# Performance work log

Measured on AMD Instinct MI355X. Metric: run time of the kernel, lower is better.

Reference implementation:

```python
import jax, jax.numpy as jnp
import numpy as np

GROUPS = 8
EPS = 1e-5


def setup_inputs() -> dict:
    key = jax.random.key(0)
    k1, k2, k3 = jax.random.split(key, 3)
    B, C, H, W = 4, 256, 64, 64
    x = jax.random.normal(k1, (B, C, H, W), dtype=jnp.float32)
    gamma = jnp.ones((C,), dtype=jnp.float32)
    beta = jnp.zeros((C,), dtype=jnp.float32)
    # conv1x1 weights flattened to [out, in]
    w_qkv = jax.random.normal(k2, (3 * C, C), dtype=jnp.float32) * (C ** -0.5)
    w_proj = jax.random.normal(k3, (C, C), dtype=jnp.float32) * (C ** -0.5)
    b_proj = jnp.zeros((C,), dtype=jnp.float32)
    return {"x": x, "gamma": gamma, "beta": beta, "w_qkv": w_qkv,
            "w_proj": w_proj, "b_proj": b_proj}


def group_norm(x, gamma, beta):
    B, C, H, W = x.shape
    xr = x.reshape(B, GROUPS, C // GROUPS, H * W)
    mu = xr.mean(axis=(2, 3), keepdims=True)
    var = xr.var(axis=(2, 3), keepdims=True)
    xn = (xr - mu) * jax.lax.rsqrt(var + EPS)
    xn = xn.reshape(B, C, H * W)
    return xn * gamma[None, :, None] + beta[None, :, None]


def reference(x, gamma, beta, w_qkv, w_proj, b_proj):
    B, C, H, W = x.shape
    N = H * W
    xn = group_norm(x, gamma, beta)               # [B, C, N]
    qkv = jnp.einsum('oc,bcn->bon', w_qkv, xn)    # [B, 3C, N]
    q, k, v = jnp.split(qkv, 3, axis=1)           # each [B, C, N]
    # attn[b, n, m] = sum_c q[b,c,n] * k[b,c,m] * C^-0.5
    scores = jnp.einsum('bcn,bcm->bnm', q, k) * (C ** -0.5)  # [B, N, N]
    attn = jax.nn.softmax(scores, axis=-1)
    # out = v @ attn^T  -> out[b,c,n] = sum_m v[b,c,m] * attn[b,n,m]
    out = jnp.einsum('bcm,bnm->bcn', v, attn)     # [B, C, N]
    y = jnp.einsum('oc,bcn->bon', w_proj, out) + b_proj[None, :, None]
    return x + y.reshape(B, C, H, W)
```

## Files before the change

kernel.cpp:

```cpp
#include <hip/hip_runtime.h>
#include <hip/hip_bf16.h>

#define BB 4
#define CC 256
#define NN 4096
#define GG 8
#define SPLITS 4
#define TKV 32
#define ITERS (NN / SPLITS / TKV)

typedef unsigned char u8;
typedef unsigned short u16;
typedef unsigned int u32;
typedef __bf16 b16x8 __attribute__((ext_vector_type(8)));
typedef float f32x4 __attribute__((ext_vector_type(4)));
typedef u32 u32x4 __attribute__((ext_vector_type(4)));
typedef u32 u32x2 __attribute__((ext_vector_type(2)));
typedef u16 u16x4 __attribute__((ext_vector_type(4)));

#define QS 0.09016844005556021f
#define FMAX 8.0f


__device__ __forceinline__ u16 f2bf(float f) {
    u32 u = __builtin_bit_cast(u32, f);
    u = (u + 0x7FFFu + ((u >> 16) & 1u)) >> 16;
    return (u16)u;
}

__device__ __forceinline__ float bf2f(u16 h) {
    return __builtin_bit_cast(float, (u32)h << 16);
}

__device__ __forceinline__ u32 pack_bf2(float a, float b) {
    float2 f; f.x = a; f.y = b;
    __hip_bfloat162 h = __float22bfloat162_rn(f);
    u32 r;
    __builtin_memcpy(&r, &h, 4);
    return r;
}

__device__ __forceinline__ float exp2_raw(float x) {
#if __has_builtin(__builtin_amdgcn_exp2f)
    return __builtin_amdgcn_exp2f(x);
#else
    float r;
    asm("v_exp_f32 %0, %1" : "=v"(r) : "v"(x));
    return r;
#endif
}

__device__ __forceinline__ b16x8 ldfrag(const u16* p) {
    u32x4 v = *reinterpret_cast<const u32x4*>(p);
    return __builtin_bit_cast(b16x8, v);
}

__device__ __forceinline__ int pk_fp8x4(float a, float b, float c, float d) {
    int r = __builtin_amdgcn_cvt_pk_fp8_f32(a, b, 0, false);
    r = __builtin_amdgcn_cvt_pk_fp8_f32(c, d, r, true);
    return r;
}

__device__ __forceinline__ long as_long(u32x2 v) { return __builtin_bit_cast(long, v); }

__device__ __forceinline__ u32 swz16(u32 v) {
    return (u32)__builtin_amdgcn_ds_swizzle((int)v, 0x401F);
}

__device__ __forceinline__ void pls32(u32& a, u32& b) {
    asm("v_permlane32_swap_b32 %0, %1" : "+v"(a), "+v"(b));
}

typedef __attribute__((address_space(1))) const unsigned int* gas_p;
typedef __attribute__((address_space(3))) unsigned int* las_p;

__device__ __forceinline__ void g2l(const u8* g, u8* l) {
    __builtin_amdgcn_global_load_lds((gas_p)g, (las_p)l, 16, 0, 0);
}

__device__ __forceinline__ void g2l16(const u16* g, u16* l) {
    __builtin_amdgcn_global_load_lds((gas_p)g, (las_p)l, 16, 0, 0);
}

__global__ void fold_w(const float* __restrict__ w_qkv, const float* __restrict__ w_proj,
                       const float* __restrict__ gamma, const float* __restrict__ beta,
                       const float* __restrict__ gsum,
                       u16* __restrict__ wqf, float* __restrict__ biasq,
                       u16* __restrict__ wpf) {
    int o = blockIdx.x;
    int b = blockIdx.y;
    int c = threadIdx.x;
    int g = c >> 5;
    const float inv = 1.f / ((CC / GG) * NN);
    float s  = gsum[(b * GG + g) * 2];
    float ss = gsum[(b * GG + g) * 2 + 1];
    float mu = s * inv;
    float rstd = rsqrtf(ss * inv - mu * mu + 1e-5f);
    float a  = gamma[c] * rstd;
    float bb = beta[c] - mu * a;
    float w = w_qkv[o * CC + c];
    size_t fe = ((size_t)((o >> 4) * 8 + (c >> 5)) * 64 + ((c & 31) >> 3) * 16 + (o & 15)) * 8 + (c & 7);
    wqf[(size_t)b * 768 * CC + fe] = f2bf(w * a);
    float part = w * bb;
    #pragma unroll
    for (int off = 32; off; off >>= 1) part += __shfl_down(part, off, 64);
    __shared__ float red[4];
    if ((threadIdx.x & 63) == 0) red[threadIdx.x >> 6] = part;
    __syncthreads();
    if (threadIdx.x == 0) biasq[b * 768 + o] = red[0] + red[1] + red[2] + red[3];
    if (b == 0 && o < CC) {
        float wp = w_proj[o * CC + c];
        wpf[fe] = f2bf(wp);
    }
}

__global__ void transpose_x(const float* __restrict__ x, u16* __restrict__ xtf,
                            float* __restrict__ gsum) {
    __shared__ float tile[64][65];
    __shared__ float red[4][4];
    int n0 = blockIdx.x * 64, c0 = blockIdx.y * 64, b = blockIdx.z;
    int t = threadIdx.x;
    int c4 = (t & 15) * 4;
    int r0 = t >> 4;
    const float* xp = x + (size_t)b * CC * NN;
    float s0 = 0.f, ss0 = 0.f, s1 = 0.f, ss1 = 0.f;
    #pragma unroll
    for (int i = 0; i < 4; ++i) {
        int row = i * 16 + r0;
        float4 v = *reinterpret_cast<const float4*>(&xp[(size_t)(c0 + row) * NN + n0 + c4]);
        tile[row][c4 + 0] = v.x; tile[row][c4 + 1] = v.y;
        tile[row][c4 + 2] = v.z; tile[row][c4 + 3] = v.w;
        float s = v.x + v.y + v.z + v.w;
        float q = v.x * v.x + v.y * v.y + v.z * v.z + v.w * v.w;
        if (i < 2) { s0 += s; ss0 += q; } else { s1 += s; ss1 += q; }
    }
    #pragma unroll
    for (int off = 32; off; off >>= 1) {
        s0 += __shfl_down(s0, off, 64); ss0 += __shfl_down(ss0, off, 64);
        s1 += __shfl_down(s1, off, 64); ss1 += __shfl_down(ss1, off, 64);
    }
    int wid = t >> 6;
    if ((t & 63) == 0) { red[wid][0] = s0; red[wid][1] = ss0; red[wid][2] = s1; red[wid][3] = ss1; }
    __syncthreads();
    if (t < 2) {
        float s  = red[0][t * 2] + red[1][t * 2] + red[2][t * 2] + red[3][t * 2];
        float ss = red[0][t * 2 + 1] + red[1][t * 2 + 1] + red[2][t * 2 + 1] + red[3][t * 2 + 1];
        int g = (c0 >> 5) + t;
        atomicAdd(&gsum[(b * GG + g) * 2], s);
        atomicAdd(&gsum[(b * GG + g) * 2 + 1], ss);
    }
    int nl = t >> 2;
    int cbq = t & 3;
    int l15 = nl & 15;
    int ntile = (n0 >> 4) + (nl >> 4);
    int kk = (c0 >> 5) + (cbq >> 1);
    u16* ob = xtf + (size_t)b * NN * CC;
    #pragma unroll
    for (int g = 0; g < 4; ++g) {
        int quad = (cbq & 1) * 2 + (g >> 1);
        int j0 = (g & 1) * 4;
        u16x4 v;
        v.x = f2bf(tile[cbq * 16 + g * 4 + 0][nl]);
        v.y = f2bf(tile[cbq * 16 + g * 4 + 1][nl]);
        v.z = f2bf(tile[cbq * 16 + g * 4 + 2][nl]);
        v.w = f2bf(tile[cbq * 16 + g * 4 + 3][nl]);
        *reinterpret_cast<u16x4*>(ob + ((size_t)(ntile * 8 + kk) * 64 + quad * 16 + l15) * 8 + j0) = v;
    }
}

__global__ void __launch_bounds__(256) qkv_gemm(const u16* __restrict__ wqf,
                                                const float* __restrict__ biasq,
                                                const u16* __restrict__ xtf,
                                                u8* __restrict__ qtf, u8* __restrict__ ktf,
                                                u8* __restrict__ vvf) {
    __shared__ u16 bx[16384];
    int b = blockIdx.z;
    int o0 = blockIdx.y * 128;
    int n0 = blockIdx.x * 64;
    int lane = threadIdx.x & 63, w = threadIdx.x >> 6;
    int l15 = lane & 15, quad = lane >> 4;
    const u16* Bg = xtf + (size_t)b * NN * CC + (size_t)n0 * 256;
    #pragma unroll
    for (int j = 0; j < 8; ++j) {
        int c = w * 8 + j;
        g2l16(Bg + (size_t)c * 512 + lane * 8, bx + (size_t)c * 512 + lane * 8);
    }
    __syncthreads();

    const u16* A = wqf + (size_t)b * 768 * CC;
    f32x4 acc[2][4] = {};
    #pragma unroll
    for (int kk = 0; kk < 8; ++kk) {
        b16x8 af[2];
        #pragma unroll
        for (int t = 0; t < 2; ++t) {
            int otile = (o0 >> 4) + w * 2 + t;
            af[t] = ldfrag(A + (size_t)(otile * 8 + kk) * 512 + lane * 8);
        }
        #pragma unroll
        for (int nt = 0; nt < 4; ++nt) {
            b16x8 bf = ldfrag(bx + (size_t)(nt * 8 + kk) * 512 + lane * 8);
            acc[0][nt] = __builtin_amdgcn_mfma_f32_16x16x32_bf16(af[0], bf, acc[0][nt], 0, 0, 0);
            acc[1][nt] = __builtin_amdgcn_mfma_f32_16x16x32_bf16(af[1], bf, acc[1][nt], 0, 0, 0);
        }
    }
    #pragma unroll
    for (int t = 0; t < 2; ++t) {
        int o_base = o0 + (w * 2 + t) * 16 + quad * 4;
        float bias[4];
        #pragma unroll
        for (int r = 0; r < 4; ++r) bias[r] = biasq[b * 768 + o_base + r];
        if (o0 < 512) {
            int oloc = (o0 < 256) ? o_base : (o_base - 256);
            u8* dst = ((o0 < 256) ? qtf : ktf) + (size_t)b * NN * CC;
            #pragma unroll
            for (int nt = 0; nt < 4; ++nt) {
                int n = n0 + nt * 16 + l15;
                int pk = pk_fp8x4(acc[t][nt][0] + bias[0], acc[t][nt][1] + bias[1],
                                  acc[t][nt][2] + bias[2], acc[t][nt][3] + bias[3]);
                size_t addr = (size_t)((n >> 4) * 4 + (oloc >> 6)) * 1024
                            + ((oloc & 31) >> 3) * 256 + (n & 15) * 16
                            + ((oloc >> 5) & 1) * 8 + (oloc & 7);
                *reinterpret_cast<u32*>(dst + addr) = (u32)pk;
            }
        } else {
            int cb = o_base - 512;
            u8* dst = vvf + (size_t)b * NN * CC;
            #pragma unroll
            for (int nt = 0; nt < 4; ++nt) {
                int kv = n0 + nt * 16 + l15;
                int pk = pk_fp8x4(acc[t][nt][0] + bias[0], acc[t][nt][1] + bias[1],
                                  acc[t][nt][2] + bias[2], acc[t][nt][3] + bias[3]);
                size_t base = (size_t)((kv >> 5) * 8 + (cb >> 5)) * 1024
                            + ((kv & 31) >> 3) * 256 + ((cb >> 4) & 1) * 8 + (kv & 7);
                #pragma unroll
                for (int r = 0; r < 4; ++r)
                    dst[base + ((cb & 15) + r) * 16] = (u8)(pk >> (r * 8));
            }
        }
    }
}

__global__ void __launch_bounds__(256, 4) flash(const u8* __restrict__ qtf,
                                                const u8* __restrict__ ktf,
                                                const u8* __restrict__ vvf,
                                                u16* __restrict__ po,
                                                float* __restrict__ lp) {
    __shared__ u8 kbuf[2][8192];
    __shared__ u8 vbuf[2][8192];
    int lin = blockIdx.x;
    int chunk = lin & 15;
    int nblk = lin >> 4;
    int b = chunk >> 2, sp = chunk & 3;
    int lane = threadIdx.x & 63, w = threadIdx.x >> 6;
    int l15 = lane & 15, quad = lane >> 4;
    int ntile = nblk * 4 + w;
    const u8* kb8 = ktf + (size_t)b * NN * CC;
    const u8* vb8 = vvf + (size_t)b * NN * CC;
    const bool qodd = (quad & 1) != 0;

    u32x4 aq[4];
    const u8* qb = qtf + (size_t)b * NN * CC + (size_t)ntile * 4096;
    #pragma unroll
    for (int s = 0; s < 4; ++s)
        aq[s] = *reinterpret_cast<const u32x4*>(qb + s * 1024 + lane * 16);

    f32x4 acco[16] = {};
    f32x4 accs[2];
    const f32x4 zz = {0.f, 0.f, 0.f, 0.f};
    float lsum = 0.f;

    const int m_beg = sp * (NN / SPLITS);

    auto stage_k = [&](int buf, int m0) {
        const u8* ks = kb8 + ((size_t)m0 << 8);
        #pragma unroll
        for (int j = 0; j < 2; ++j) {
            int idx = w * 2 + j;
            g2l(ks + idx * 1024 + lane * 16, &kbuf[buf][idx * 1024]);
        }
    };
    auto stage_v = [&](int buf, int m0) {
        const u8* vs = vb8 + ((size_t)m0 << 8);
        #pragma unroll
        for (int j = 0; j < 2; ++j) {
            int idx = w * 2 + j;
            g2l(vs + idx * 1024 + lane * 16, &vbuf[buf][idx * 1024]);
        }
    };
    auto qk_tile = [&](const u8* kc) {
        __builtin_amdgcn_s_setprio(1);
        #pragma unroll
        for (int s = 0; s < 4; ++s) {
            long qlo = as_long(u32x2{aq[s].x, aq[s].y});
            long qhi = as_long(u32x2{aq[s].z, aq[s].w});
            #pragma unroll
            for (int mm = 0; mm < 2; ++mm) {
                u32x4 kf = *reinterpret_cast<const u32x4*>(kc + (size_t)(mm * 4 + s) * 1024 + lane * 16);
                accs[mm] = __builtin_amdgcn_mfma_f32_16x16x32_fp8_fp8(
                    as_long(u32x2{kf.x, kf.y}), qlo, (s == 0) ? zz : accs[mm], 0, 0, 0);
                accs[mm] = __builtin_amdgcn_mfma_f32_16x16x32_fp8_fp8(
                    as_long(u32x2{kf.z, kf.w}), qhi, accs[mm], 0, 0, 0);
            }
        }
        __builtin_amdgcn_s_setprio(0);
    };
    auto exch = [&](int pa, int pb) -> long {
        u32 a = (u32)pa, bm = (u32)pb;
        u32 ax = swz16(a), bx = swz16(bm);
        pls32(a, bm);
        pls32(ax, bx);
        u32 blo = qodd ? bx : a;
        u32 bhi = qodd ? bm : ax;
        return as_long(u32x2{blo, bhi});
    };

    stage_k(0, m_beg);
    stage_v(0, m_beg);
    stage_k(1, m_beg + TKV);
    __syncthreads();
    qk_tile(&kbuf[0][0]);
    __syncthreads();

    for (int it = 0; it < ITERS; ++it) {
        int cur = it & 1;
        int pk[2];
        #pragma unroll
        for (int mm = 0; mm < 2; ++mm) {
            float e0 = exp2_raw(fmaf(accs[mm][0], QS, -FMAX));
            float e1 = exp2_raw(fmaf(accs[mm][1], QS, -FMAX));
            float e2 = exp2_raw(fmaf(accs[mm][2], QS, -FMAX));
            float e3 = exp2_raw(fmaf(accs[mm][3], QS, -FMAX));
            lsum += (e0 + e1) + (e2 + e3);
            pk[mm] = pk_fp8x4(e0, e1, e2, e3);
        }
        if (it + 1 < ITERS) qk_tile(&kbuf[cur ^ 1][0]);
        if (it + 2 < ITERS) stage_k(cur, m_beg + (it + 2) * TKV);
        if (it + 1 < ITERS) stage_v(cur ^ 1, m_beg + (it + 1) * TKV);
        const u8* vc = &vbuf[cur][0];
        long bop = exch(pk[0], pk[1]);
        __builtin_amdgcn_s_setprio(1);
        #pragma unroll
        for (int c2 = 0; c2 < 8; ++c2) {
            u32x4 vf = *reinterpret_cast<const u32x4*>(vc + (size_t)c2 * 1024 + lane * 16);
            acco[c2 * 2]     = __builtin_amdgcn_mfma_f32_16x16x32_fp8_fp8(
                as_long(u32x2{vf.x, vf.y}), bop, acco[c2 * 2], 0, 0, 0);
            acco[c2 * 2 + 1] = __builtin_amdgcn_mfma_f32_16x16x32_fp8_fp8(
                as_long(u32x2{vf.z, vf.w}), bop, acco[c2 * 2 + 1], 0, 0, 0);
        }
        __builtin_amdgcn_s_setprio(0);
        __syncthreads();
    }
    u16* pochunk = po + ((size_t)(sp * BB + b) * 256 + ntile) * 4096;
    #pragma unroll
    for (int ct = 0; ct < 16; ++ct) {
        u32x2 st;
        st.x = pack_bf2(acco[ct][0], acco[ct][1]);
        st.y = pack_bf2(acco[ct][2], acco[ct][3]);
        *reinterpret_cast<u32x2*>(pochunk + (size_t)(ct * 64 + quad * 16 + l15) * 4) = st;
    }
    lsum += __shfl_xor(lsum, 16, 64);
    lsum += __shfl_xor(lsum, 32, 64);
    if (lane < 16)
        lp[(size_t)(sp * BB + b) * NN + ntile * 16 + l15] = lsum;
}

__global__ void __launch_bounds__(512) proj(const u16* __restrict__ wpf,
                                            const float* __restrict__ b_proj,
                                            const u16* __restrict__ po,
                                            const float* __restrict__ lp,
                                            const float* __restrict__ x,
                                            float* __restrict__ out) {
    __shared__ u16 bO[16384];
    int b = blockIdx.y, n0 = blockIdx.x * 64;
    int t = threadIdx.x;
    {
        int u = t & 127, ntl = t >> 7;
        int nb = (n0 >> 4) + ntl;
        int a = u & 7;
        int cblk = u >> 3;
        float accn[2][16] = {};
        float lsum2[2] = {};
        #pragma unroll
        for (int s = 0; s < SPLITS; ++s) {
            const u16* src = po + (((size_t)(s * BB + b) * 256 + nb) * 4096)
                           + cblk * 256 + a * 8;
            #pragma unroll
            for (int q4 = 0; q4 < 4; ++q4) {
                u16 s16[8];
                *reinterpret_cast<u32x4*>(s16) = *reinterpret_cast<const u32x4*>(src + q4 * 64);
                #pragma unroll
                for (int k = 0; k < 8; ++k)
                    accn[k >> 2][q4 * 4 + (k & 3)] += bf2f(s16[k]);
            }
            lsum2[0] += lp[(size_t)(s * BB + b) * NN + nb * 16 + a * 2];
            lsum2[1] += lp[(size_t)(s * BB + b) * NN + nb * 16 + a * 2 + 1];
        }
        #pragma unroll
        for (int nsel = 0; nsel < 2; ++nsel) {
            float inv = 1.f / lsum2[nsel];
            int row = a * 2 + nsel;
            #pragma unroll
            for (int h = 0; h < 2; ++h) {
                u16 outv[8];
                #pragma unroll
                for (int j = 0; j < 8; ++j) outv[j] = f2bf(accn[nsel][h * 8 + j] * inv);
                int kk = cblk >> 1, quad_f = (cblk & 1) * 2 + h;
                size_t off = ((size_t)(ntl * 8 + kk) * 64 + quad_f * 16 + row) * 8;
                *reinterpret_cast<u32x4*>(bO + off) = *reinterpret_cast<const u32x4*>(outv);
            }
        }
    }
    __syncthreads();
    int lane = t & 63, w = t >> 6;
    int l15 = lane & 15, quad = lane >> 4;
    f32x4 acc2[2][4] = {};
    #pragma unroll
    for (int kk = 0; kk < 8; ++kk) {
        b16x8 af[2];
        #pragma unroll
        for (int tt = 0; tt < 2; ++tt) {
            int otile = w * 2 + tt;
            af[tt] = ldfrag(wpf + (size_t)(otile * 8 + kk) * 512 + lane * 8);
        }
        #pragma unroll
        for (int nt = 0; nt < 4; ++nt) {
            b16x8 bf = ldfrag(bO + (size_t)(nt * 8 + kk) * 512 + lane * 8);
            acc2[0][nt] = __builtin_amdgcn_mfma_f32_16x16x32_bf16(af[0], bf, acc2[0][nt], 0, 0, 0);
            acc2[1][nt] = __builtin_amdgcn_mfma_f32_16x16x32_bf16(af[1], bf, acc2[1][nt], 0, 0, 0);
        }
    }
    #pragma unroll
    for (int tt = 0; tt < 2; ++tt) {
        int o_base = (w * 2 + tt) * 16 + quad * 4;
        #pragma unroll
        for (int nt = 0; nt < 4; ++nt) {
            int n = n0 + nt * 16 + l15;
            #pragma unroll
            for (int r = 0; r < 4; ++r) {
                int o = o_base + r;
                size_t idx = ((size_t)(b * CC + o)) * NN + n;
                out[idx] = acc2[tt][nt][r] + b_proj[o] + x[idx];
            }
        }
    }
}

extern "C" void kernel_launch(void* const* d_in, const int* in_sizes, int n_in,
                              void* d_out, int out_size, void* d_ws, size_t ws_size,
                              hipStream_t stream) {
    const float* x      = (const float*)d_in[0];
    const float* gamma  = (const float*)d_in[1];
    const float* beta   = (const float*)d_in[2];
    const float* w_qkv  = (const float*)d_in[3];
    const float* w_proj = (const float*)d_in[4];
    const float* b_proj = (const float*)d_in[5];
    float* out = (float*)d_out;

    char* p = (char*)d_ws;
    float* gsum  = (float*)p; p += 256;
    float* biasq = (float*)p; p += (size_t)BB * 768 * sizeof(float);
    u16* wqf = (u16*)p; p += (size_t)BB * 768 * CC * 2;
    u16* wpf = (u16*)p; p += (size_t)CC * CC * 2;
    u16* xtf = (u16*)p; p += (size_t)BB * NN * CC * 2;
    u8* qtf8 = (u8*)p; p += (size_t)BB * NN * CC;
    u8* ktf8 = (u8*)p; p += (size_t)BB * NN * CC;
    u8* vvf8 = (u8*)p; p += (size_t)BB * NN * CC;
    u16* po = (u16*)p; p += (size_t)SPLITS * BB * NN * CC * 2;
    float* lp = (float*)p; p += (size_t)SPLITS * BB * NN * sizeof(float);
    (void)ws_size; (void)in_sizes; (void)n_in; (void)out_size;

    (void)hipMemsetAsync(gsum, 0, BB * GG * 2 * sizeof(float), stream);
    transpose_x<<<dim3(NN / 64, CC / 64, BB), 256, 0, stream>>>(x, xtf, gsum);
    fold_w<<<dim3(768, BB), 256, 0, stream>>>(w_qkv, w_proj, gamma, beta, gsum, wqf, biasq, wpf);
    qkv_gemm<<<dim3(NN / 64, 6, BB), 256, 0, stream>>>(wqf, biasq, xtf, qtf8, ktf8, vvf8);
    flash<<<(NN / 64) * SPLITS * BB, 256, 0, stream>>>(qtf8, ktf8, vvf8, po, lp);
    proj<<<dim3(NN / 64, BB), 512, 0, stream>>>(wpf, b_proj, po, lp, x, out);
}
```

Before: 173.5 us.

## Use 16x16x128 scaled FP8 MFMA for QK scores with new Q/K layout

Replaces the sixteen 16x16x32 fp8 MFMAs per QK tile with four 16x16x128 f8f6f4 scaled MFMAs, with unit scales. The Q/K global layout written by the projection kernel changes so each lane reads 32 contiguous bytes per 128-channel chunk. The aim is fewer MFMA issues and higher MFMA throughput on gfx950. The new LDS read pattern (row stride 128 bytes) may cause bank conflicts.

```diff
diff --git a/kernel.cpp b/kernel.cpp
--- a/kernel.cpp
+++ b/kernel.cpp
@@ -17,6 +17,7 @@
 typedef u32 u32x4 __attribute__((ext_vector_type(4)));
 typedef u32 u32x2 __attribute__((ext_vector_type(2)));
 typedef u16 u16x4 __attribute__((ext_vector_type(4)));
+typedef int i32x8 __attribute__((ext_vector_type(8)));
 
 #define QS 0.09016844005556021f
 #define FMAX 8.0f
@@ -62,6 +63,17 @@
 }
 
 __device__ __forceinline__ long as_long(u32x2 v) { return __builtin_bit_cast(long, v); }
+
+__device__ __forceinline__ i32x8 cat8(u32x4 a, u32x4 b) {
+    i32x8 r;
+    r[0] = (int)a.x; r[1] = (int)a.y; r[2] = (int)a.z; r[3] = (int)a.w;
+    r[4] = (int)b.x; r[5] = (int)b.y; r[6] = (int)b.z; r[7] = (int)b.w;
+    return r;
+}
+
+__device__ __forceinline__ f32x4 mfma_qk128(i32x8 a, i32x8 b, f32x4 c) {
+    return __builtin_amdgcn_mfma_scale_f32_16x16x128_f8f6f4(a, b, c, 0, 0, 0, 127, 0, 127);
+}
 
 __device__ __forceinline__ u32 swz16(u32 v) {
     return (u32)__builtin_amdgcn_ds_swizzle((int)v, 0x401F);
@@ -218,9 +230,8 @@
                 int n = n0 + nt * 16 + l15;
                 int pk = pk_fp8x4(acc[t][nt][0] + bias[0], acc[t][nt][1] + bias[1],
                                   acc[t][nt][2] + bias[2], acc[t][nt][3] + bias[3]);
-                size_t addr = (size_t)((n >> 4) * 4 + (oloc >> 6)) * 1024
-                            + ((oloc & 31) >> 3) * 256 + (n & 15) * 16
-                            + ((oloc >> 5) & 1) * 8 + (oloc & 7);
+                size_t addr = (size_t)(n >> 4) * 4096 + (size_t)(oloc >> 7) * 2048
+                            + (size_t)(n & 15) * 128 + (oloc & 127);
                 *reinterpret_cast<u32*>(dst + addr) = (u32)pk;
             }
         } else {
@@ -259,11 +270,17 @@
     const u8* vb8 = vvf + (size_t)b * NN * CC;
     const bool qodd = (quad & 1) != 0;
 
-    u32x4 aq[4];
-    const u8* qb = qtf + (size_t)b * NN * CC + (size_t)ntile * 4096;
-    #pragma unroll
-    for (int s = 0; s < 4; ++s)
-        aq[s] = *reinterpret_cast<const u32x4*>(qb + s * 1024 + lane * 16);
+    i32x8 qop[2];
+    {
+        const u8* qp = qtf + (size_t)b * NN * CC + (size_t)ntile * 4096
+                     + (size_t)l15 * 128 + (size_t)quad * 32;
+        u32x4 q0 = *reinterpret_cast<const u32x4*>(qp);
+        u32x4 q1 = *reinterpret_cast<const u32x4*>(qp + 16);
+        u32x4 q2 = *reinterpret_cast<const u32x4*>(qp + 2048);
+        u32x4 q3 = *reinterpret_cast<const u32x4*>(qp + 2048 + 16);
+        qop[0] = cat8(q0, q1);
+        qop[1] = cat8(q2, q3);
+    }
 
     f32x4 acco[16] = {};
     f32x4 accs[2];
@@ -290,18 +307,18 @@
     };
     auto qk_tile = [&](const u8* kc) {
         __builtin_amdgcn_s_setprio(1);
-        #pragma unroll
-        for (int s = 0; s < 4; ++s) {
-            long qlo = as_long(u32x2{aq[s].x, aq[s].y});
-            long qhi = as_long(u32x2{aq[s].z, aq[s].w});
-            #pragma unroll
-            for (int mm = 0; mm < 2; ++mm) {
-                u32x4 kf = *reinterpret_cast<const u32x4*>(kc + (size_t)(mm * 4 + s) * 1024 + lane * 16);
-                accs[mm] = __builtin_amdgcn_mfma_f32_16x16x32_fp8_fp8(
-                    as_long(u32x2{kf.x, kf.y}), qlo, (s == 0) ? zz : accs[mm], 0, 0, 0);
-                accs[mm] = __builtin_amdgcn_mfma_f32_16x16x32_fp8_fp8(
-                    as_long(u32x2{kf.z, kf.w}), qhi, accs[mm], 0, 0, 0);
-            }
+        const u8* kp = kc + (size_t)l15 * 128 + (size_t)quad * 32;
+        #pragma unroll
+        for (int mm = 0; mm < 2; ++mm) {
+            f32x4 acc = zz;
+            #pragma unroll
+            for (int cc = 0; cc < 2; ++cc) {
+                const u8* p = kp + mm * 4096 + cc * 2048;
+                u32x4 k0 = *reinterpret_cast<const u32x4*>(p);
+                u32x4 k1 = *reinterpret_cast<const u32x4*>(p + 16);
+                acc = mfma_qk128(cat8(k0, k1), qop[cc], acc);
+            }
+            accs[mm] = acc;
         }
         __builtin_amdgcn_s_setprio(0);
     };
```

Measured after the change: 174.7 us. No clear change (+0.7%).
